# Optimization experiments

Measured on AMD Instinct MI355X. Metric: run time of the kernel, lower is better.

The kernel has to match this reference:

```python
import jax, jax.numpy as jnp
import numpy as np
from jax import lax

B_, L_, IN, H, LYR = 8, 512, 64, 512, 4
ED, N, DC, DTR = 2 * H, 16, 4, 32  # d_inner, d_state, d_conv, dt_rank (mamba.py defaults)


def setup_inputs() -> dict:
    key = jax.random.key(0)
    ks = iter(jax.random.split(key, 24))
    def nrm(shape, s=0.02):
        return jax.random.normal(next(ks), shape, jnp.float32) * s
    A_log = jnp.tile(jnp.log(jnp.arange(1, N + 1, dtype=jnp.float32))[None, None, :], (LYR, ED, 1))
    return {
        "x": jax.random.normal(next(ks), (B_, L_, IN), jnp.float32),
        "w_in": nrm((H, IN)), "b_in": jnp.zeros((H,), jnp.float32),
        "ln1_w": jnp.ones((H,), jnp.float32), "ln1_b": jnp.zeros((H,), jnp.float32),
        "norm_w": jnp.ones((LYR, H), jnp.float32),
        "in_proj_w": nrm((LYR, 2 * ED, H)),
        "conv_w": nrm((LYR, ED, DC)), "conv_b": jnp.zeros((LYR, ED), jnp.float32),
        "x_proj_w": nrm((LYR, DTR + 2 * N, ED)),
        "dt_proj_w": nrm((LYR, ED, DTR)), "dt_proj_b": nrm((LYR, ED), 0.1),
        "A_log": A_log, "D": jnp.ones((LYR, ED), jnp.float32),
        "out_proj_w": nrm((LYR, H, ED)),
        "w_ref": nrm((H, H)), "b_ref": jnp.zeros((H,), jnp.float32),
        "ln2_w": jnp.ones((H,), jnp.float32), "ln2_b": jnp.zeros((H,), jnp.float32),
        "w_o1": nrm((H // 2, H)), "b_o1": jnp.zeros((H // 2,), jnp.float32),
        "w_o2": nrm((1, H // 2)), "b_o2": jnp.zeros((1,), jnp.float32),
    }


def _ln(x, w, b):
    mu = x.mean(-1, keepdims=True)
    xc = x - mu
    return xc * lax.rsqrt((xc * xc).mean(-1, keepdims=True) + 1e-5) * w + b


def _rms(x, w):
    return x * lax.rsqrt((x * x).mean(-1, keepdims=True) + 1e-5) * w


def _scan(dA, dBu, C):
    # dA, dBu: (B, L, ED, N); C: (B, L, N) -> y: (B, L, ED)
    def step(h, t):
        dA_t, dBu_t, c_t = t
        h = dA_t * h + dBu_t
        return h, jnp.einsum('ben,bn->be', h, c_t)
    h0 = jnp.zeros((dA.shape[0], ED, N), dA.dtype)
    _, ys = lax.scan(step, h0, (dA.swapaxes(0, 1), dBu.swapaxes(0, 1), C.swapaxes(0, 1)))
    return ys.swapaxes(0, 1)


def _mixer(x, in_w, cw, cb, xp_w, dt_w, dt_b, A_log, D, out_w):
    xz = x @ in_w.T                               # (B, L, 2*ED)
    xc, z = jnp.split(xz, 2, axis=-1)
    # depthwise causal conv1d, kernel DC, left-pad DC-1
    xt = lax.conv_general_dilated(xc.swapaxes(1, 2), cw[:, None, :], (1,), [(DC - 1, 0)],
                                  dimension_numbers=('NCH', 'OIH', 'NCH'), feature_group_count=ED)
    u = jax.nn.silu(xt.swapaxes(1, 2) + cb)       # (B, L, ED)
    dbc = u @ xp_w.T                              # (B, L, DTR + 2N)
    delta = jax.nn.softplus(dbc[..., :DTR] @ dt_w.T + dt_b)   # (B, L, ED)
    Bm, Cm = dbc[..., DTR:DTR + N], dbc[..., DTR + N:]
    A = -jnp.exp(A_log)                           # (ED, N)
    dA = jnp.exp(delta[..., None] * A)            # (B, L, ED, N)
    dBu = delta[..., None] * Bm[:, :, None, :] * u[..., None]
    y = _scan(dA, dBu, Cm) + D * u
    return (y * jax.nn.silu(z)) @ out_w.T


def reference(x, w_in, b_in, ln1_w, ln1_b, norm_w, in_proj_w, conv_w, conv_b, x_proj_w,
              dt_proj_w, dt_proj_b, A_log, D, out_proj_w, w_ref, b_ref, ln2_w, ln2_b,
              w_o1, b_o1, w_o2, b_o2):
    h = jax.nn.gelu(_ln(x @ w_in.T + b_in, ln1_w, ln1_b), approximate=False)
    hm = h
    for l in range(LYR):  # residual Mamba blocks (pre-RMSNorm)
        hm = hm + _mixer(_rms(hm, norm_w[l]), in_proj_w[l], conv_w[l], conv_b[l], x_proj_w[l],
                         dt_proj_w[l], dt_proj_b[l], A_log[l], D[l], out_proj_w[l])
    h = h + hm
    h = jax.nn.gelu(_ln(h @ w_ref.T + b_ref, ln2_w, ln2_b), approximate=False)  # dropout=eval
    h = jax.nn.gelu(h @ w_o1.T + b_o1, approximate=False)
    y = jax.nn.sigmoid(h @ w_o2.T + b_o2)
    return y[..., 0]
```

## Files before the change

### kernel.cpp

```cpp
#include <hip/hip_runtime.h>
#include <math.h>


#define BL 4096
#define H_ 512
#define ED_ 1024
#define N_ 16
#define DTR_ 32
#define CCH 16
#define TCH 32
#define L2E 1.44269504088896340736f

typedef unsigned short u16;
typedef unsigned int u32;
typedef __attribute__((ext_vector_type(8))) short short8;
typedef __attribute__((ext_vector_type(4))) float f32x4;

__device__ __forceinline__ float fexp2_(float x){ return __builtin_amdgcn_exp2f(x); }
__device__ __forceinline__ float geluf_(float x){ return 0.5f*x*(1.f+erff(x*0.70710678118654752f)); }
__device__ __forceinline__ float softplusf_(float x){ return (x>20.f)? x : log1pf(expf(x)); }
__device__ __forceinline__ float siluf_(float x){ return x/(1.f+fexp2_(-L2E*x)); }

__device__ __forceinline__ void split_bf16(float x, u16& hi, u16& lo){
  u32 u = __float_as_uint(x);
  u32 r = (u + 0x7fffu + ((u>>16)&1u)) >> 16;
  hi = (u16)r;
  float hf = __uint_as_float(r<<16);
  float rem = x - hf;
  u32 v = __float_as_uint(rem);
  lo = (u16)((v + 0x7fffu + ((v>>16)&1u)) >> 16);
}

__device__ __forceinline__ float block_reduce_sum(float v, float* sm){
  #pragma unroll
  for (int o=32;o>0;o>>=1) v += __shfl_down(v,o,64);
  if ((threadIdx.x&63)==0) sm[threadIdx.x>>6]=v;
  __syncthreads();
  float r = sm[0]+sm[1]+sm[2]+sm[3];
  __syncthreads();
  return r;
}

#define GLOAD_LDS16(g, l) __builtin_amdgcn_global_load_lds( \
    (const __attribute__((address_space(1))) u32*)(g), \
    (__attribute__((address_space(3))) u32*)(l), 16, 0, 0)

#define LDSBUF ((128+64)*64)
template<int ACT, int HAS_BIAS, int HAS_RES>
__device__ __forceinline__ void stage_tile(
  const u16* __restrict__ A, int lda, const u16* __restrict__ B, int ldb,
  int m0, int n0, int K, int kt, int tid, u16* lbase)
{
  #pragma unroll
  for (int i=0;i<4;i++){
    int c = tid + i*256;
    int r = c>>3, s = c&7;
    int j = s ^ (r&7);
    int col = (j<4) ? (kt + (j<<3)) : (K + kt + ((j-4)<<3));
    GLOAD_LDS16(A + (size_t)(m0+r)*lda + col, lbase + c*8);
  }
  #pragma unroll
  for (int i=0;i<2;i++){
    int c = tid + i*256;
    int r = c>>3, s = c&7;
    int j = s ^ (r&7);
    int col = (j<4) ? (kt + (j<<3)) : (K + kt + ((j-4)<<3));
    GLOAD_LDS16(B + (size_t)(n0+r)*ldb + col, lbase + 128*64 + c*8);
  }
}

template<int ACT, int HAS_BIAS, int HAS_RES>
__global__ __launch_bounds__(256) void mfma_gemm(
  const u16* __restrict__ A, int lda,
  const u16* __restrict__ B, int ldb,
  float* __restrict__ C, int ldc,
  const float* __restrict__ bias,
  const float* __restrict__ res,
  int K)
{
  __shared__ u16 lds[2*LDSBUF];
  int tid = threadIdx.x;
  int lane = tid & 63, w = tid >> 6;
  int wr = w >> 1, wc = w & 1;
  int nbx = gridDim.x;
  int nb  = nbx * gridDim.y;
  int lid = blockIdx.y*nbx + blockIdx.x;
  int cpx = nb >> 3;
  int swz = (lid & 7)*cpx + (lid >> 3);
  int m0 = (swz / nbx)*128, n0 = (swz % nbx)*64;

  f32x4 acc[4][2] = {};
  const int NK = K >> 5;
  stage_tile<ACT,HAS_BIAS,HAS_RES>(A,lda,B,ldb,m0,n0,K,0,tid,&lds[0]);
  __syncthreads();
  int cur = 0;
  for (int t=0; t<NK; t++){
    if (t+1 < NK)
      stage_tile<ACT,HAS_BIAS,HAS_RES>(A,lda,B,ldb,m0,n0,K,(t+1)<<5,tid,&lds[(cur^1)*LDSBUF]);
    const char* lb = (const char*)&lds[cur*LDSBUF];
    int kb = (lane>>4)<<4;
    short8 ah[4], al[4], bh[2], bl[2];
    #pragma unroll
    for (int fr=0; fr<4; fr++){
      int row = wr*64 + fr*16 + (lane&15);
      int sw = (row&7)<<4;
      ah[fr] = *(const short8*)(lb + row*128 + (kb ^ sw));
      al[fr] = *(const short8*)(lb + row*128 + ((64+kb) ^ sw));
    }
    #pragma unroll
    for (int fc=0; fc<2; fc++){
      int row = wc*32 + fc*16 + (lane&15);
      int sw = (row&7)<<4;
      bh[fc] = *(const short8*)(lb + 128*128 + row*128 + (kb ^ sw));
      bl[fc] = *(const short8*)(lb + 128*128 + row*128 + ((64+kb) ^ sw));
    }
    #pragma unroll
    for (int fr=0; fr<4; fr++)
      #pragma unroll
      for (int fc=0; fc<2; fc++)
        acc[fr][fc] = __builtin_amdgcn_mfma_f32_16x16x32_bf16(ah[fr], bh[fc], acc[fr][fc], 0,0,0);
    #pragma unroll
    for (int fr=0; fr<4; fr++)
      #pragma unroll
      for (int fc=0; fc<2; fc++)
        acc[fr][fc] = __builtin_amdgcn_mfma_f32_16x16x32_bf16(al[fr], bh[fc], acc[fr][fc], 0,0,0);
    #pragma unroll
    for (int fr=0; fr<4; fr++)
      #pragma unroll
      for (int fc=0; fc<2; fc++)
        acc[fr][fc] = __builtin_amdgcn_mfma_f32_16x16x32_bf16(ah[fr], bl[fc], acc[fr][fc], 0,0,0);
    __syncthreads();
    cur ^= 1;
  }
  #pragma unroll
  for (int fr=0; fr<4; fr++){
    #pragma unroll
    for (int fc=0; fc<2; fc++){
      #pragma unroll
      for (int j=0;j<4;j++){
        int m = m0 + wr*64 + fr*16 + (lane>>4)*4 + j;
        int n = n0 + wc*32 + fc*16 + (lane&15);
        float v = acc[fr][fc][j];
        if (HAS_BIAS) v += bias[n];
        if (ACT==1) v = geluf_(v);
        if (HAS_RES) v += res[(size_t)m*ldc + n];
        C[(size_t)m*ldc + n] = v;
      }
    }
  }
}

__global__ __launch_bounds__(256) void wconv_kernel(
  const float* __restrict__ in, u16* __restrict__ out, int kbits)
{
  size_t i = (size_t)blockIdx.x*256 + threadIdx.x;
  int K = 1<<kbits;
  size_t n = i >> kbits;
  int k = (int)(i & (size_t)(K-1));
  u16 hi, lo; split_bf16(in[i], hi, lo);
  size_t ob = n << (kbits+1);
  out[ob + k] = hi; out[ob + K + k] = lo;
}

template<int ACT, int HAS_BIAS, int HAS_RES>
__global__ __launch_bounds__(256) void gemm_bt(
  const float* __restrict__ A, int lda,
  const float* __restrict__ B, int ldb,
  float* __restrict__ C, int ldc,
  const float* __restrict__ bias,
  const float* __restrict__ res,
  int K)
{
  __shared__ float As[16][65];
  __shared__ float Bs[16][65];
  int tid = threadIdx.x;
  int tx = tid & 15, ty = tid >> 4;
  int m0 = blockIdx.y*64, n0 = blockIdx.x*64;
  float acc[4][4] = {};
  for (int kt=0; kt<K; kt+=16){
    #pragma unroll
    for (int i=0;i<4;i++){
      int idx = tid + i*256;
      int r = idx>>4, c = idx&15;
      As[c][r] = A[(size_t)(m0+r)*lda + kt + c];
      Bs[c][r] = B[(size_t)(n0+r)*ldb + kt + c];
    }
    __syncthreads();
    #pragma unroll
    for (int k=0;k<16;k++){
      float a[4],b[4];
      #pragma unroll
      for (int i=0;i<4;i++) a[i]=As[k][ty*4+i];
      #pragma unroll
      for (int j=0;j<4;j++) b[j]=Bs[k][tx*4+j];
      #pragma unroll
      for (int i=0;i<4;i++)
        #pragma unroll
        for (int j=0;j<4;j++)
          acc[i][j] = fmaf(a[i], b[j], acc[i][j]);
    }
    __syncthreads();
  }
  #pragma unroll
  for (int i=0;i<4;i++){
    int m = m0 + ty*4 + i;
    #pragma unroll
    for (int j=0;j<4;j++){
      int n = n0 + tx*4 + j;
      float v = acc[i][j];
      if (HAS_BIAS) v += bias[n];
      if (ACT==1) v = geluf_(v);
      else if (ACT==2) v = softplusf_(v);
      if (HAS_RES) v += res[(size_t)m*ldc + n];
      C[(size_t)m*ldc + n] = v;
    }
  }
}

__global__ __launch_bounds__(256) void xproj_kernel(
  const float* __restrict__ u, const float* __restrict__ xw,
  float* __restrict__ dbc)
{
  int t = threadIdx.x;
  int l = t & 63, wv = t >> 6;
  int m0 = blockIdx.x * 8;
  f32x4 ur[8][4];
  #pragma unroll
  for (int m=0;m<8;m++){
    const f32x4* up = (const f32x4*)(u + (size_t)(m0+m)*1024 + (l<<4));
    #pragma unroll
    for (int q=0;q<4;q++) ur[m][q] = up[q];
  }
  #pragma unroll 2
  for (int j=0;j<16;j++){
    int n = wv*16 + j;
    const f32x4* wp = (const f32x4*)(xw + (size_t)n*1024 + (l<<4));
    f32x4 w4[4];
    #pragma unroll
    for (int q=0;q<4;q++) w4[q] = wp[q];
    float p[8];
    #pragma unroll
    for (int m=0;m<8;m++){
      float s = 0.f;
      #pragma unroll
      for (int q=0;q<4;q++){
        s = fmaf(ur[m][q][0], w4[q][0], s);
        s = fmaf(ur[m][q][1], w4[q][1], s);
        s = fmaf(ur[m][q][2], w4[q][2], s);
        s = fmaf(ur[m][q][3], w4[q][3], s);
      }
      #pragma unroll
      for (int o=32;o>0;o>>=1) s += __shfl_xor(s, o, 64);
      p[m] = s;
    }
    if (l == 0){
      #pragma unroll
      for (int m=0;m<8;m++) dbc[(size_t)(m0+m)*64 + n] = p[m];
    }
  }
}

__global__ __launch_bounds__(256) void dt_flat_kernel(
  const float* __restrict__ dbc, const float* __restrict__ dt_w,
  const float* __restrict__ dt_b, float* __restrict__ delta)
{
  int e  = (blockIdx.x & 3)*256 + threadIdx.x;
  int mg = blockIdx.x >> 2;
  f32x4 w[8];
  const f32x4* wp = (const f32x4*)(dt_w + (size_t)e*DTR_);
  #pragma unroll
  for (int q=0;q<8;q++) w[q] = wp[q];
  float bias = dt_b[e];
  #pragma unroll
  for (int i=0;i<4;i++){
    int m = mg*4 + i;
    const f32x4* dp = (const f32x4*)(dbc + (size_t)m*64);
    float s = 0.f;
    #pragma unroll
    for (int q=0;q<8;q++){
      f32x4 d = dp[q];
      #pragma unroll
      for (int j=0;j<4;j++) s = fmaf(d[j], w[q][j], s);
    }
    delta[(size_t)m*ED_ + e] = softplusf_(s + bias);
  }
}

__global__ __launch_bounds__(256) void ln_gelu_kernel(
  const float* __restrict__ in, const float* __restrict__ w, const float* __restrict__ b,
  float* __restrict__ out1, float* __restrict__ out2)
{
  __shared__ float sm[4];
  size_t row = blockIdx.x;
  const float* xr = in + row*H_;
  int t = threadIdx.x;
  float x0 = xr[t], x1 = xr[t+256];
  float mu = block_reduce_sum(x0+x1, sm) * (1.f/512.f);
  float c0 = x0-mu, c1 = x1-mu;
  float var = block_reduce_sum(c0*c0+c1*c1, sm) * (1.f/512.f);
  float rs = rsqrtf(var + 1e-5f);
  float y0 = geluf_(c0*rs*w[t]     + b[t]);
  float y1 = geluf_(c1*rs*w[t+256] + b[t+256]);
  out1[row*H_+t] = y0; out1[row*H_+t+256] = y1;
  if (out2){ out2[row*H_+t] = y0; out2[row*H_+t+256] = y1; }
}

__global__ __launch_bounds__(256) void ln_gelu_b3_kernel(
  const float* __restrict__ in, const float* __restrict__ w, const float* __restrict__ b,
  u16* __restrict__ out)
{
  __shared__ float sm[4];
  size_t row = blockIdx.x;
  const float* xr = in + row*H_;
  int t = threadIdx.x;
  float x0 = xr[t], x1 = xr[t+256];
  float mu = block_reduce_sum(x0+x1, sm) * (1.f/512.f);
  float c0 = x0-mu, c1 = x1-mu;
  float var = block_reduce_sum(c0*c0+c1*c1, sm) * (1.f/512.f);
  float rs = rsqrtf(var + 1e-5f);
  float y0 = geluf_(c0*rs*w[t]     + b[t]);
  float y1 = geluf_(c1*rs*w[t+256] + b[t+256]);
  u16 hi,lo;
  split_bf16(y0,hi,lo); out[row*1024 + t]     = hi; out[row*1024 + 512 + t]     = lo;
  split_bf16(y1,hi,lo); out[row*1024 + t+256] = hi; out[row*1024 + 512 + t+256] = lo;
}

__global__ __launch_bounds__(256) void rms_b3_kernel(
  const float* __restrict__ in, const float* __restrict__ w, u16* __restrict__ out)
{
  __shared__ float sm[4];
  size_t row = blockIdx.x;
  const float* xr = in + row*H_;
  int t = threadIdx.x;
  float x0 = xr[t], x1 = xr[t+256];
  float ss = block_reduce_sum(x0*x0+x1*x1, sm) * (1.f/512.f);
  float rs = rsqrtf(ss + 1e-5f);
  float y0 = x0*rs*w[t], y1 = x1*rs*w[t+256];
  u16 hi,lo;
  split_bf16(y0,hi,lo); out[row*1024 + t]     = hi; out[row*1024 + 512 + t]     = lo;
  split_bf16(y1,hi,lo); out[row*1024 + t+256] = hi; out[row*1024 + 512 + t+256] = lo;
}

__global__ __launch_bounds__(256) void add_b3_kernel(
  const float* __restrict__ a, const float* __restrict__ b, u16* __restrict__ out)
{
  size_t i = (size_t)blockIdx.x*256 + threadIdx.x;
  float v = a[i] + b[i];
  size_t r = i >> 9, c = i & 511;
  u16 hi,lo; split_bf16(v,hi,lo);
  out[r*1024 + c] = hi; out[r*1024 + 512 + c] = lo;
}

__global__ __launch_bounds__(256) void conv_silu_kernel(
  const float* __restrict__ xz, const float* __restrict__ cw, const float* __restrict__ cb,
  float* __restrict__ u)
{
  int token = blockIdx.x;
  int e = blockIdx.y*256 + threadIdx.x;
  int b = token >> 9, t = token & 511;
  float acc = cb[e];
  #pragma unroll
  for (int k=0;k<4;k++){
    int tt = t - 3 + k;
    if (tt >= 0) acc = fmaf(cw[e*4+k], xz[((size_t)((b<<9)|tt))*2048 + e], acc);
  }
  u[(size_t)token*ED_ + e] = siluf_(acc);
}


__global__ __launch_bounds__(256) void scan_pass1(
  const float* __restrict__ delta, const float* __restrict__ u,
  const float* __restrict__ dbc, const float* __restrict__ A_log,
  float* __restrict__ dts_out, float* __restrict__ Sb)
{
  int gid = blockIdx.x*256 + threadIdx.x;
  int e = gid & 1023;
  int c = (gid >> 10) & (CCH-1);
  int b = gid >> 14;
  int p = (b<<10) | e;
  float al2[16];
  {
    const f32x4* ar = (const f32x4*)(A_log + e*16);
    #pragma unroll
    for (int q=0;q<4;q++){
      f32x4 av = ar[q];
      #pragma unroll
      for (int j=0;j<4;j++) al2[q*4+j] = -fexp2_(av[j]*L2E)*L2E;
    }
  }
  int tokbase = (b<<9) + c*TCH;
  const float* dptr = delta + (size_t)tokbase*ED_ + e;
  const float* uptr = u     + (size_t)tokbase*ED_ + e;
  const f32x4* bc   = (const f32x4*)(dbc + (size_t)tokbase*64 + 32);
  float S[16];
  #pragma unroll
  for (int n=0;n<16;n++) S[n]=0.f;
  float dts = 0.f;
  float dt = dptr[0], ut = uptr[0];
  f32x4 Bv[4];
  #pragma unroll
  for (int q=0;q<4;q++) Bv[q] = bc[q];
  #pragma unroll 4
  for (int t=0;t<TCH;t++){
    int tn = (t+1 < TCH) ? t+1 : t;
    float ndt = dptr[(size_t)tn*ED_];
    float nut = uptr[(size_t)tn*ED_];
    f32x4 nBv[4];
    #pragma unroll
    for (int q=0;q<4;q++) nBv[q] = bc[tn*16+q];
    float du = dt*ut;
    dts += dt;
    #pragma unroll
    for (int q=0;q<4;q++)
      #pragma unroll
      for (int j=0;j<4;j++){
        int n = q*4+j;
        float da = fexp2_(dt*al2[n]);
        S[n] = fmaf(da, S[n], du*Bv[q][j]);
      }
    dt = ndt; ut = nut;
    #pragma unroll
    for (int q=0;q<4;q++) Bv[q] = nBv[q];
  }
  f32x4* sp = (f32x4*)(Sb + ((size_t)(c*8192 + p))*16);
  #pragma unroll
  for (int q=0;q<4;q++){
    f32x4 sv; sv[0]=S[q*4]; sv[1]=S[q*4+1]; sv[2]=S[q*4+2]; sv[3]=S[q*4+3];
    sp[q] = sv;
  }
  dts_out[c*8192 + p] = dts;
}

__global__ __launch_bounds__(256) void scan_pass2(
  const float* __restrict__ dts, float* __restrict__ Sb,
  const float* __restrict__ A_log)
{
  int i = blockIdx.x*256 + threadIdx.x;
  int n = i & 15;
  int p = i >> 4;
  int e = p & 1023;
  float al2 = -fexp2_(A_log[e*16+n]*L2E)*L2E;
  float h = 0.f;
  #pragma unroll
  for (int c=0;c<CCH;c++){
    size_t off = (size_t)c*(8192*16) + i;
    float S = Sb[off];
    Sb[off] = h;
    float P = fexp2_(al2 * dts[c*8192 + p]);
    h = fmaf(P, h, S);
  }
}

__global__ __launch_bounds__(256) void scan_pass3(
  const float* __restrict__ delta, const float* __restrict__ u,
  const float* __restrict__ dbc, const float* __restrict__ xz,
  const float* __restrict__ A_log, const float* __restrict__ D,
  const float* __restrict__ hin,
  u16* __restrict__ g3)
{
  int gid = blockIdx.x*256 + threadIdx.x;
  int e = gid & 1023;
  int c = (gid >> 10) & (CCH-1);
  int b = gid >> 14;
  int p = (b<<10) | e;
  float al2[16];
  {
    const f32x4* ar = (const f32x4*)(A_log + e*16);
    #pragma unroll
    for (int q=0;q<4;q++){
      f32x4 av = ar[q];
      #pragma unroll
      for (int j=0;j<4;j++) al2[q*4+j] = -fexp2_(av[j]*L2E)*L2E;
    }
  }
  float h[16];
  {
    const f32x4* hp = (const f32x4*)(hin + ((size_t)(c*8192 + p))*16);
    #pragma unroll
    for (int q=0;q<4;q++){
      f32x4 hv = hp[q];
      #pragma unroll
      for (int j=0;j<4;j++) h[q*4+j] = hv[j];
    }
  }
  float de = D[e];
  int tokbase = (b<<9) + c*TCH;
  const float* dptr = delta + (size_t)tokbase*ED_ + e;
  const float* uptr = u     + (size_t)tokbase*ED_ + e;
  const f32x4* bc   = (const f32x4*)(dbc + (size_t)tokbase*64 + 32);
  const float* zptr = xz + (size_t)tokbase*2048 + 1024 + e;
  u16* gp = g3 + (size_t)tokbase*4096 + e;
  float dt = dptr[0], ut = uptr[0], zt = zptr[0];
  f32x4 Bv[4], Cv[4];
  #pragma unroll
  for (int q=0;q<4;q++){ Bv[q] = bc[q]; Cv[q] = bc[4+q]; }
  #pragma unroll 4
  for (int t=0;t<TCH;t++){
    int tn = (t+1 < TCH) ? t+1 : t;
    float ndt = dptr[(size_t)tn*ED_];
    float nut = uptr[(size_t)tn*ED_];
    float nzt = zptr[(size_t)tn*2048];
    f32x4 nBv[4], nCv[4];
    #pragma unroll
    for (int q=0;q<4;q++){ nBv[q] = bc[tn*16+q]; nCv[q] = bc[tn*16+4+q]; }
    float du = dt*ut;
    float yq[4] = {0.f,0.f,0.f,0.f};
    #pragma unroll
    for (int q=0;q<4;q++)
      #pragma unroll
      for (int j=0;j<4;j++){
        int n = q*4+j;
        float da = fexp2_(dt*al2[n]);
        h[n] = fmaf(da, h[n], du*Bv[q][j]);
        yq[q] = fmaf(h[n], Cv[q][j], yq[q]);
      }
    float y = (yq[0]+yq[1]) + (yq[2]+yq[3]);
    float gv = (y + de*ut) * siluf_(zt);
    u16 hi,lo; split_bf16(gv,hi,lo);
    gp[(size_t)t*4096] = hi; gp[(size_t)t*4096 + 1024] = lo;
    dt = ndt; ut = nut; zt = nzt;
    #pragma unroll
    for (int q=0;q<4;q++){ Bv[q] = nBv[q]; Cv[q] = nCv[q]; }
  }
}

__global__ __launch_bounds__(64) void head_kernel(
  const float* __restrict__ t2, const float* __restrict__ w, const float* __restrict__ b,
  float* __restrict__ out)
{
  int token = blockIdx.x;
  int lane = threadIdx.x;
  float s = 0.f;
  #pragma unroll
  for (int i=0;i<4;i++){
    int c = lane + i*64;
    s = fmaf(t2[(size_t)token*256 + c], w[c], s);
  }
  #pragma unroll
  for (int o=32;o>0;o>>=1) s += __shfl_down(s,o,64);
  if (lane==0) out[token] = 1.f/(1.f+expf(-(s + b[0])));
}

extern "C" void kernel_launch(void* const* d_in, const int* in_sizes, int n_in,
                              void* d_out, int out_size, void* d_ws, size_t ws_size,
                              hipStream_t stream) {
  const float* x         = (const float*)d_in[0];
  const float* w_in      = (const float*)d_in[1];
  const float* b_in      = (const float*)d_in[2];
  const float* ln1_w     = (const float*)d_in[3];
  const float* ln1_b     = (const float*)d_in[4];
  const float* norm_w    = (const float*)d_in[5];
  const float* in_proj_w = (const float*)d_in[6];
  const float* conv_w    = (const float*)d_in[7];
  const float* conv_b    = (const float*)d_in[8];
  const float* x_proj_w  = (const float*)d_in[9];
  const float* dt_proj_w = (const float*)d_in[10];
  const float* dt_proj_b = (const float*)d_in[11];
  const float* A_log     = (const float*)d_in[12];
  const float* Dp        = (const float*)d_in[13];
  const float* out_proj_w= (const float*)d_in[14];
  const float* w_ref     = (const float*)d_in[15];
  const float* b_ref     = (const float*)d_in[16];
  const float* ln2_w     = (const float*)d_in[17];
  const float* ln2_b     = (const float*)d_in[18];
  const float* w_o1      = (const float*)d_in[19];
  const float* b_o1      = (const float*)d_in[20];
  const float* w_o2      = (const float*)d_in[21];
  const float* b_o2      = (const float*)d_in[22];
  float* out = (float*)d_out;

  float* ws   = (float*)d_ws;
  float* h0   = ws;
  float* hm   = h0   + (size_t)BL*H_;
  float* t512 = hm   + (size_t)BL*H_;
  float* xz   = t512 + (size_t)BL*H_;
  float* u    = xz   + (size_t)BL*2048;
  float* dbc  = u    + (size_t)BL*ED_;
  float* delta= dbc  + (size_t)BL*64;
  float* t2   = delta+ (size_t)BL*ED_;

  u16* a3u  = (u16*)t512;
  u16* wb3u = (u16*)t2;
  u16* wt3u = (u16*)hm;
  u16* g3u  = (u16*)xz;
  float* Sb   = t512;
  float* dts  = t2;

  gemm_bt<0,1,0><<<dim3(8,64),256,0,stream>>>(x,64, w_in,64, t512,H_, b_in,nullptr, 64);
  ln_gelu_kernel<<<BL,256,0,stream>>>(t512, ln1_w, ln1_b, h0, hm);

  for (int l=0;l<4;l++){
    rms_b3_kernel<<<BL,256,0,stream>>>(hm, norm_w + l*H_, a3u);
    wconv_kernel<<<2048*512/256,256,0,stream>>>(in_proj_w + (size_t)l*2048*H_, wb3u, 9);
    mfma_gemm<0,0,0><<<dim3(32,32),256,0,stream>>>(a3u,1024, wb3u,1024, xz,2048, nullptr,nullptr, 512);
    conv_silu_kernel<<<dim3(BL,4),256,0,stream>>>(xz, conv_w + l*ED_*4, conv_b + l*ED_, u);
    xproj_kernel<<<BL/8,256,0,stream>>>(u, x_proj_w + (size_t)l*64*ED_, dbc);
    dt_flat_kernel<<<BL,256,0,stream>>>(dbc, dt_proj_w + (size_t)l*ED_*DTR_, dt_proj_b + l*ED_, delta);
    scan_pass1<<<8192*CCH/256,256,0,stream>>>(delta, u, dbc, A_log + (size_t)l*ED_*N_, dts, Sb);
    scan_pass2<<<8192*16/256,256,0,stream>>>(dts, Sb, A_log + (size_t)l*ED_*N_);
    scan_pass3<<<8192*CCH/256,256,0,stream>>>(delta, u, dbc, xz, A_log + (size_t)l*ED_*N_, Dp + l*ED_, Sb, g3u);
    wconv_kernel<<<512*1024/256,256,0,stream>>>(out_proj_w + (size_t)l*H_*ED_, wb3u, 10);
    mfma_gemm<0,0,1><<<dim3(8,32),256,0,stream>>>(g3u,4096, wb3u,2048, hm,512, nullptr, hm, 1024);
  }

  add_b3_kernel<<<BL*H_/256,256,0,stream>>>(h0, hm, a3u);
  wconv_kernel<<<512*512/256,256,0,stream>>>(w_ref, wt3u, 9);
  mfma_gemm<0,1,0><<<dim3(8,32),256,0,stream>>>(a3u,1024, wt3u,1024, u,512, b_ref, nullptr, 512);
  ln_gelu_b3_kernel<<<BL,256,0,stream>>>(u, ln2_w, ln2_b, a3u);
  wconv_kernel<<<256*512/256,256,0,stream>>>(w_o1, wt3u, 9);
  mfma_gemm<1,1,0><<<dim3(4,32),256,0,stream>>>(a3u,1024, wt3u,1024, t2,256, b_o1, nullptr, 512);
  head_kernel<<<BL,64,0,stream>>>(t2, w_o2, b_o2, out);
}
```

Measured before the change: 835.1 us.

## Fuse dt projection into scan passes and add 128x128 in_proj GEMM tile

Removes the separate dt_flat kernel and its BL x ED delta buffer. Each scan pass now computes delta per token as a 32-wide dot product plus softplus, using weights held in registers, which cuts delta writes and reads at the cost of doing that arithmetic twice (once in pass1, once in pass3). The in_proj GEMM also gets a new 128x128 tile kernel with a 4x4 MFMA fragment per wave, meant to give more reuse per LDS load, though it raises register pressure and leaves fewer blocks in the grid.

```diff
diff --git a/kernel.cpp b/kernel.cpp
--- a/kernel.cpp
+++ b/kernel.cpp
@@ -46,7 +46,6 @@
     (__attribute__((address_space(3))) u32*)(l), 16, 0, 0)
 
 #define LDSBUF ((128+64)*64)
-template<int ACT, int HAS_BIAS, int HAS_RES>
 __device__ __forceinline__ void stage_tile(
   const u16* __restrict__ A, int lda, const u16* __restrict__ B, int ldb,
   int m0, int n0, int K, int kt, int tid, u16* lbase)
@@ -91,12 +90,12 @@
 
   f32x4 acc[4][2] = {};
   const int NK = K >> 5;
-  stage_tile<ACT,HAS_BIAS,HAS_RES>(A,lda,B,ldb,m0,n0,K,0,tid,&lds[0]);
+  stage_tile(A,lda,B,ldb,m0,n0,K,0,tid,&lds[0]);
   __syncthreads();
   int cur = 0;
   for (int t=0; t<NK; t++){
     if (t+1 < NK)
-      stage_tile<ACT,HAS_BIAS,HAS_RES>(A,lda,B,ldb,m0,n0,K,(t+1)<<5,tid,&lds[(cur^1)*LDSBUF]);
+      stage_tile(A,lda,B,ldb,m0,n0,K,(t+1)<<5,tid,&lds[(cur^1)*LDSBUF]);
     const char* lb = (const char*)&lds[cur*LDSBUF];
     int kb = (lane>>4)<<4;
     short8 ah[4], al[4], bh[2], bl[2];
@@ -150,6 +149,103 @@
   }
 }
 
+#define LDSBUF_BIG (256*64)
+__device__ __forceinline__ void stage_tile_big(
+  const u16* __restrict__ A, int lda, const u16* __restrict__ B, int ldb,
+  int m0, int n0, int K, int kt, int tid, u16* lbase)
+{
+  #pragma unroll
+  for (int i=0;i<4;i++){
+    int c = tid + i*256;
+    int r = c>>3, s = c&7;
+    int j = s ^ (r&7);
+    int col = (j<4) ? (kt + (j<<3)) : (K + kt + ((j-4)<<3));
+    GLOAD_LDS16(A + (size_t)(m0+r)*lda + col, lbase + c*8);
+  }
+  #pragma unroll
+  for (int i=0;i<4;i++){
+    int c = tid + i*256;
+    int r = c>>3, s = c&7;
+    int j = s ^ (r&7);
+    int col = (j<4) ? (kt + (j<<3)) : (K + kt + ((j-4)<<3));
+    GLOAD_LDS16(B + (size_t)(n0+r)*ldb + col, lbase + 128*64 + c*8);
+  }
+}
+
+__global__ __launch_bounds__(256) void mfma_gemm_big(
+  const u16* __restrict__ A, int lda,
+  const u16* __restrict__ B, int ldb,
+  float* __restrict__ C, int ldc,
+  int K)
+{
+  __shared__ u16 lds[2*LDSBUF_BIG];
+  int tid = threadIdx.x;
+  int lane = tid & 63, w = tid >> 6;
+  int wr = w >> 1, wc = w & 1;
+  int nbx = gridDim.x;
+  int nb  = nbx * gridDim.y;
+  int lid = blockIdx.y*nbx + blockIdx.x;
+  int cpx = nb >> 3;
+  int swz = (lid & 7)*cpx + (lid >> 3);
+  int m0 = (swz / nbx)*128, n0 = (swz % nbx)*128;
+
+  f32x4 acc[4][4] = {};
+  const int NK = K >> 5;
+  stage_tile_big(A,lda,B,ldb,m0,n0,K,0,tid,&lds[0]);
+  __syncthreads();
+  int cur = 0;
+  for (int t=0; t<NK; t++){
+    if (t+1 < NK)
+      stage_tile_big(A,lda,B,ldb,m0,n0,K,(t+1)<<5,tid,&lds[(cur^1)*LDSBUF_BIG]);
+    const char* lb = (const char*)&lds[cur*LDSBUF_BIG];
+    int kb = (lane>>4)<<4;
+    short8 ah[4], al[4], bh[4], bl[4];
+    #pragma unroll
+    for (int fr=0; fr<4; fr++){
+      int row = wr*64 + fr*16 + (lane&15);
+      int sw = (row&7)<<4;
+      ah[fr] = *(const short8*)(lb + row*128 + (kb ^ sw));
+      al[fr] = *(const short8*)(lb + row*128 + ((64+kb) ^ sw));
+    }
+    #pragma unroll
+    for (int fc=0; fc<4; fc++){
+      int row = wc*64 + fc*16 + (lane&15);
+      int sw = (row&7)<<4;
+      bh[fc] = *(const short8*)(lb + 16384 + row*128 + (kb ^ sw));
+      bl[fc] = *(const short8*)(lb + 16384 + row*128 + ((64+kb) ^ sw));
+    }
+    #pragma unroll
+    for (int fr=0; fr<4; fr++)
+      #pragma unroll
+      for (int fc=0; fc<4; fc++)
+        acc[fr][fc] = __builtin_amdgcn_mfma_f32_16x16x32_bf16(ah[fr], bh[fc], acc[fr][fc], 0,0,0);
+    #pragma unroll
+    for (int fr=0; fr<4; fr++)
+      #pragma unroll
+      for (int fc=0; fc<4; fc++)
+        acc[fr][fc] = __builtin_amdgcn_mfma_f32_16x16x32_bf16(al[fr], bh[fc], acc[fr][fc], 0,0,0);
+    #pragma unroll
+    for (int fr=0; fr<4; fr++)
+      #pragma unroll
+      for (int fc=0; fc<4; fc++)
+        acc[fr][fc] = __builtin_amdgcn_mfma_f32_16x16x32_bf16(ah[fr], bl[fc], acc[fr][fc], 0,0,0);
+    __syncthreads();
+    cur ^= 1;
+  }
+  #pragma unroll
+  for (int fr=0; fr<4; fr++){
+    #pragma unroll
+    for (int fc=0; fc<4; fc++){
+      #pragma unroll
+      for (int j=0;j<4;j++){
+        int m = m0 + wr*64 + fr*16 + (lane>>4)*4 + j;
+        int n = n0 + wc*64 + fc*16 + (lane&15);
+        C[(size_t)m*ldc + n] = acc[fr][fc][j];
+      }
+    }
+  }
+}
+
 __global__ __launch_bounds__(256) void wconv_kernel(
   const float* __restrict__ in, u16* __restrict__ out, int kbits)
 {
@@ -257,32 +353,6 @@
       #pragma unroll
       for (int m=0;m<8;m++) dbc[(size_t)(m0+m)*64 + n] = p[m];
     }
-  }
-}
-
-__global__ __launch_bounds__(256) void dt_flat_kernel(
-  const float* __restrict__ dbc, const float* __restrict__ dt_w,
-  const float* __restrict__ dt_b, float* __restrict__ delta)
-{
-  int e  = (blockIdx.x & 3)*256 + threadIdx.x;
-  int mg = blockIdx.x >> 2;
-  f32x4 w[8];
-  const f32x4* wp = (const f32x4*)(dt_w + (size_t)e*DTR_);
-  #pragma unroll
-  for (int q=0;q<8;q++) w[q] = wp[q];
-  float bias = dt_b[e];
-  #pragma unroll
-  for (int i=0;i<4;i++){
-    int m = mg*4 + i;
-    const f32x4* dp = (const f32x4*)(dbc + (size_t)m*64);
-    float s = 0.f;
-    #pragma unroll
-    for (int q=0;q<8;q++){
-      f32x4 d = dp[q];
-      #pragma unroll
-      for (int j=0;j<4;j++) s = fmaf(d[j], w[q][j], s);
-    }
-    delta[(size_t)m*ED_ + e] = softplusf_(s + bias);
   }
 }
 
@@ -368,9 +438,22 @@
 }
 
 
+__device__ __forceinline__ float dt_dot(const f32x4* __restrict__ row,
+                                        const f32x4* __restrict__ wd, float bias){
+  float s = 0.f;
+  #pragma unroll
+  for (int q=0;q<8;q++){
+    f32x4 d = row[q];
+    #pragma unroll
+    for (int j=0;j<4;j++) s = fmaf(d[j], wd[q][j], s);
+  }
+  return softplusf_(s + bias);
+}
+
 __global__ __launch_bounds__(256) void scan_pass1(
-  const float* __restrict__ delta, const float* __restrict__ u,
-  const float* __restrict__ dbc, const float* __restrict__ A_log,
+  const float* __restrict__ u, const float* __restrict__ dbc,
+  const float* __restrict__ A_log,
+  const float* __restrict__ dt_w, const float* __restrict__ dt_b,
   float* __restrict__ dts_out, float* __restrict__ Sb)
 {
   int gid = blockIdx.x*256 + threadIdx.x;
@@ -388,26 +471,32 @@
       for (int j=0;j<4;j++) al2[q*4+j] = -fexp2_(av[j]*L2E)*L2E;
     }
   }
+  f32x4 wd[8];
+  {
+    const f32x4* wp = (const f32x4*)(dt_w + (size_t)e*DTR_);
+    #pragma unroll
+    for (int q=0;q<8;q++) wd[q] = wp[q];
+  }
+  float bias = dt_b[e];
   int tokbase = (b<<9) + c*TCH;
-  const float* dptr = delta + (size_t)tokbase*ED_ + e;
-  const float* uptr = u     + (size_t)tokbase*ED_ + e;
-  const f32x4* bc   = (const f32x4*)(dbc + (size_t)tokbase*64 + 32);
+  const float* uptr = u + (size_t)tokbase*ED_ + e;
+  const f32x4* bcrow = (const f32x4*)(dbc + (size_t)tokbase*64);
   float S[16];
   #pragma unroll
   for (int n=0;n<16;n++) S[n]=0.f;
   float dts = 0.f;
-  float dt = dptr[0], ut = uptr[0];
+  float ut = uptr[0];
   f32x4 Bv[4];
   #pragma unroll
-  for (int q=0;q<4;q++) Bv[q] = bc[q];
+  for (int q=0;q<4;q++) Bv[q] = bcrow[8+q];
   #pragma unroll 4
   for (int t=0;t<TCH;t++){
     int tn = (t+1 < TCH) ? t+1 : t;
-    float ndt = dptr[(size_t)tn*ED_];
     float nut = uptr[(size_t)tn*ED_];
     f32x4 nBv[4];
     #pragma unroll
-    for (int q=0;q<4;q++) nBv[q] = bc[tn*16+q];
+    for (int q=0;q<4;q++) nBv[q] = bcrow[tn*16+8+q];
+    float dt = dt_dot(bcrow + t*16, wd, bias);
     float du = dt*ut;
     dts += dt;
     #pragma unroll
@@ -418,7 +507,7 @@
         float da = fexp2_(dt*al2[n]);
         S[n] = fmaf(da, S[n], du*Bv[q][j]);
       }
-    dt = ndt; ut = nut;
+    ut = nut;
     #pragma unroll
     for (int q=0;q<4;q++) Bv[q] = nBv[q];
   }
@@ -452,9 +541,11 @@
 }
 
 __global__ __launch_bounds__(256) void scan_pass3(
-  const float* __restrict__ delta, const float* __restrict__ u,
-  const float* __restrict__ dbc, const float* __restrict__ xz,
-  const float* __restrict__ A_log, const float* __restrict__ D,
+  const float* __restrict__ u, const float* __restrict__ dbc,
+  const float* __restrict__ xz,
+  const float* __restrict__ A_log,
+  const float* __restrict__ dt_w, const float* __restrict__ dt_b,
+  const float* __restrict__ D,
   const float* __restrict__ hin,
   u16* __restrict__ g3)
 {
@@ -473,6 +564,13 @@
       for (int j=0;j<4;j++) al2[q*4+j] = -fexp2_(av[j]*L2E)*L2E;
     }
   }
+  f32x4 wd[8];
+  {
+    const f32x4* wp = (const f32x4*)(dt_w + (size_t)e*DTR_);
+    #pragma unroll
+    for (int q=0;q<8;q++) wd[q] = wp[q];
+  }
+  float bias = dt_b[e];
   float h[16];
   {
     const f32x4* hp = (const f32x4*)(hin + ((size_t)(c*8192 + p))*16);
@@ -485,24 +583,23 @@
   }
   float de = D[e];
   int tokbase = (b<<9) + c*TCH;
-  const float* dptr = delta + (size_t)tokbase*ED_ + e;
-  const float* uptr = u     + (size_t)tokbase*ED_ + e;
-  const f32x4* bc   = (const f32x4*)(dbc + (size_t)tokbase*64 + 32);
+  const float* uptr = u + (size_t)tokbase*ED_ + e;
+  const f32x4* bcrow = (const f32x4*)(dbc + (size_t)tokbase*64);
   const float* zptr = xz + (size_t)tokbase*2048 + 1024 + e;
   u16* gp = g3 + (size_t)tokbase*4096 + e;
-  float dt = dptr[0], ut = uptr[0], zt = zptr[0];
+  float ut = uptr[0], zt = zptr[0];
   f32x4 Bv[4], Cv[4];
   #pragma unroll
-  for (int q=0;q<4;q++){ Bv[q] = bc[q]; Cv[q] = bc[4+q]; }
+  for (int q=0;q<4;q++){ Bv[q] = bcrow[8+q]; Cv[q] = bcrow[12+q]; }
   #pragma unroll 4
   for (int t=0;t<TCH;t++){
     int tn = (t+1 < TCH) ? t+1 : t;
-    float ndt = dptr[(size_t)tn*ED_];
     float nut = uptr[(size_t)tn*ED_];
     float nzt = zptr[(size_t)tn*2048];
     f32x4 nBv[4], nCv[4];
     #pragma unroll
-    for (int q=0;q<4;q++){ nBv[q] = bc[tn*16+q]; nCv[q] = bc[tn*16+4+q]; }
+    for (int q=0;q<4;q++){ nBv[q] = bcrow[tn*16+8+q]; nCv[q] = bcrow[tn*16+12+q]; }
+    float dt = dt_dot(bcrow + t*16, wd, bias);
     float du = dt*ut;
     float yq[4] = {0.f,0.f,0.f,0.f};
     #pragma unroll
@@ -518,7 +615,7 @@
     float gv = (y + de*ut) * siluf_(zt);
     u16 hi,lo; split_bf16(gv,hi,lo);
     gp[(size_t)t*4096] = hi; gp[(size_t)t*4096 + 1024] = lo;
-    dt = ndt; ut = nut; zt = nzt;
+    ut = nut; zt = nzt;
     #pragma unroll
     for (int q=0;q<4;q++){ Bv[q] = nBv[q]; Cv[q] = nCv[q]; }
   }
@@ -576,8 +673,9 @@
   float* xz   = t512 + (size_t)BL*H_;
   float* u    = xz   + (size_t)BL*2048;
   float* dbc  = u    + (size_t)BL*ED_;
-  float* delta= dbc  + (size_t)BL*64;
-  float* t2   = delta+ (size_t)BL*ED_;
+  float* spare= dbc  + (size_t)BL*64;
+  float* t2   = spare+ (size_t)BL*ED_;
+  (void)spare;
 
   u16* a3u  = (u16*)t512;
   u16* wb3u = (u16*)t2;
@@ -592,13 +690,14 @@
   for (int l=0;l<4;l++){
     rms_b3_kernel<<<BL,256,0,stream>>>(hm, norm_w + l*H_, a3u);
     wconv_kernel<<<2048*512/256,256,0,stream>>>(in_proj_w + (size_t)l*2048*H_, wb3u, 9);
-    mfma_gemm<0,0,0><<<dim3(32,32),256,0,stream>>>(a3u,1024, wb3u,1024, xz,2048, nullptr,nullptr, 512);
+    mfma_gemm_big<<<dim3(16,32),256,0,stream>>>(a3u,1024, wb3u,1024, xz,2048, 512);
     conv_silu_kernel<<<dim3(BL,4),256,0,stream>>>(xz, conv_w + l*ED_*4, conv_b + l*ED_, u);
     xproj_kernel<<<BL/8,256,0,stream>>>(u, x_proj_w + (size_t)l*64*ED_, dbc);
-    dt_flat_kernel<<<BL,256,0,stream>>>(dbc, dt_proj_w + (size_t)l*ED_*DTR_, dt_proj_b + l*ED_, delta);
-    scan_pass1<<<8192*CCH/256,256,0,stream>>>(delta, u, dbc, A_log + (size_t)l*ED_*N_, dts, Sb);
+    scan_pass1<<<8192*CCH/256,256,0,stream>>>(u, dbc, A_log + (size_t)l*ED_*N_,
+        dt_proj_w + (size_t)l*ED_*DTR_, dt_proj_b + l*ED_, dts, Sb);
     scan_pass2<<<8192*16/256,256,0,stream>>>(dts, Sb, A_log + (size_t)l*ED_*N_);
-    scan_pass3<<<8192*CCH/256,256,0,stream>>>(delta, u, dbc, xz, A_log + (size_t)l*ED_*N_, Dp + l*ED_, Sb, g3u);
+    scan_pass3<<<8192*CCH/256,256,0,stream>>>(u, dbc, xz, A_log + (size_t)l*ED_*N_,
+        dt_proj_w + (size_t)l*ED_*DTR_, dt_proj_b + l*ED_, Dp + l*ED_, Sb, g3u);
     wconv_kernel<<<512*1024/256,256,0,stream>>>(out_proj_w + (size_t)l*H_*ED_, wb3u, 10);
     mfma_gemm<0,0,1><<<dim3(8,32),256,0,stream>>>(g3u,4096, wb3u,2048, hm,512, nullptr, hm, 1024);
   }
```

Result: slower. 895.1 us (+7.2%).
